# Optimization experiments

Measured on AMD Instinct MI355X. Metric: run time of the kernel, lower is better.

The kernel has to match this reference:

```python
import jax, jax.numpy as jnp
import numpy as np

B, S, D, H = 2, 1024, 1024, 16
DH = D // H
EPS = 1e-5

def _ln(x, g, b):
    m = jnp.mean(x, axis=-1, keepdims=True)
    v = jnp.mean((x - m) ** 2, axis=-1, keepdims=True)
    return (x - m) / jnp.sqrt(v + EPS) * g + b

def setup_inputs() -> dict:
    key = jax.random.key(0)
    ks = jax.random.split(key, 5)
    scale = 1.0 / np.sqrt(D)
    return {
        "id": jax.random.normal(ks[0], (B, S, D), dtype=jnp.float32),
        "Wq": jax.random.uniform(ks[1], (D, D), jnp.float32, -scale, scale),
        "Wk": jax.random.uniform(ks[2], (D, D), jnp.float32, -scale, scale),
        "Wv": jax.random.uniform(ks[3], (D, D), jnp.float32, -scale, scale),
        "g0": jnp.ones((D,), jnp.float32), "b0": jnp.zeros((D,), jnp.float32),
        "g1": jnp.ones((D,), jnp.float32), "b1": jnp.zeros((D,), jnp.float32),
        "g2": jnp.ones((D,), jnp.float32), "b2": jnp.zeros((D,), jnp.float32),
    }

def reference(id, Wq, Wk, Wv, g0, b0, g1, b1, g2, b2):
    residual = id
    id_ln = _ln(id, g0, b0)
    # torch Linear: x @ W.T ; split heads along last dim, cat along batch
    q = (id_ln @ Wq.T).reshape(B, S, H, DH)
    k = (id_ln @ Wk.T).reshape(B, S, H, DH)
    v = (id_ln @ Wv.T).reshape(B, S, H, DH)
    scores = jnp.einsum('bqhd,bkhd->bhqk', q, k) / np.sqrt(DH)
    A = jax.nn.softmax(scores, axis=-1)                      # [B,H,S,S]
    O = jnp.einsum('bhqk,bkhd->bqhd', A, v).reshape(B, S, D)  # merge heads
    left = _ln(id_ln + O, g1, b1)
    right = _ln(residual + O, g2, b2)
    out = left + right
    # torch layout of A is [(H*B), S, S] with head-major ordering
    A_out = jnp.transpose(A, (1, 0, 2, 3)).reshape(H * B, S, S)
    return (out, A_out)
```

## Files before the change

kernel.cpp:

```cpp
#include <hip/hip_runtime.h>

namespace {

constexpr int B = 2, S = 1024, D = 1024, H = 16, DH = 64;
constexpr int M = B * S;
constexpr float EPS = 1e-5f;

using bf16x8 = __attribute__((ext_vector_type(8))) short;
using bf16x4 = __attribute__((ext_vector_type(4))) short;
using f32x4  = __attribute__((ext_vector_type(4))) float;

typedef const __attribute__((address_space(1))) void* gptr_t;
typedef __attribute__((address_space(3))) void* lptr_t;

__device__ __forceinline__ unsigned short f2bf(float f) {
    union { float f; unsigned u; } v{f};
    unsigned r = v.u + 0x7fffu + ((v.u >> 16) & 1u);
    return (unsigned short)(r >> 16);
}

__device__ __forceinline__ float bflo(unsigned u) {
    union { unsigned u; float f; } v{u << 16}; return v.f;
}
__device__ __forceinline__ float bfhi(unsigned u) {
    union { unsigned u; float f; } v{u & 0xffff0000u}; return v.f;
}

__device__ __forceinline__ float wave_sum(float v) {
#pragma unroll
    for (int off = 32; off > 0; off >>= 1) v += __shfl_down(v, off, 64);
    return v;
}

__global__ __launch_bounds__(256) void cvt_w_kernel(
    const float* __restrict__ Wq, const float* __restrict__ Wk,
    const float* __restrict__ Wv, unsigned short* __restrict__ Wb)
{
    const float* src = (blockIdx.z == 0) ? Wq : (blockIdx.z == 1) ? Wk : Wv;
    const size_t i = ((size_t)blockIdx.x * 256 + threadIdx.x) * 4;
    float4 f = *reinterpret_cast<const float4*>(src + i);
    ushort4 h;
    h.x = f2bf(f.x); h.y = f2bf(f.y); h.z = f2bf(f.z); h.w = f2bf(f.w);
    *reinterpret_cast<ushort4*>(Wb + (size_t)blockIdx.z * D * D + i) = h;
}

__global__ __launch_bounds__(256) void ln0_kernel(
    const float* __restrict__ x, const float* __restrict__ g,
    const float* __restrict__ bt, float* __restrict__ y,
    unsigned short* __restrict__ yb)
{
    __shared__ float sm[8];
    __shared__ float stats[2];
    const int row = blockIdx.x;
    const int t = threadIdx.x;
    const float4 v = reinterpret_cast<const float4*>(x + (size_t)row * D)[t];
    float s  = v.x + v.y + v.z + v.w;
    float ss = v.x*v.x + v.y*v.y + v.z*v.z + v.w*v.w;
    s = wave_sum(s); ss = wave_sum(ss);
    const int lane = t & 63, wid = t >> 6;
    if (lane == 0) { sm[wid] = s; sm[4 + wid] = ss; }
    __syncthreads();
    if (t == 0) {
        float S1 = sm[0] + sm[1] + sm[2] + sm[3];
        float S2 = sm[4] + sm[5] + sm[6] + sm[7];
        float m  = S1 * (1.0f / D);
        float var = S2 * (1.0f / D) - m * m;
        stats[0] = m; stats[1] = rsqrtf(var + EPS);
    }
    __syncthreads();
    const float m = stats[0], r = stats[1];
    const float4 gv = reinterpret_cast<const float4*>(g)[t];
    const float4 bv = reinterpret_cast<const float4*>(bt)[t];
    float4 o;
    o.x = (v.x - m) * r * gv.x + bv.x;
    o.y = (v.y - m) * r * gv.y + bv.y;
    o.z = (v.z - m) * r * gv.z + bv.z;
    o.w = (v.w - m) * r * gv.w + bv.w;
    reinterpret_cast<float4*>(y + (size_t)row * D)[t] = o;
    ushort4 h; h.x = f2bf(o.x); h.y = f2bf(o.y); h.z = f2bf(o.z); h.w = f2bf(o.w);
    *reinterpret_cast<ushort4*>(yb + (size_t)row * D + t * 4) = h;
}

__global__ __launch_bounds__(256) void qkv_mfma_kernel(
    const unsigned short* __restrict__ idln, const unsigned short* __restrict__ Wb,
    unsigned short* __restrict__ q, unsigned short* __restrict__ k,
    unsigned short* __restrict__ vT)
{
    __shared__ unsigned short As[128 * 32];
    __shared__ unsigned short Bs[128 * 32];
    const int zi = blockIdx.z;
    const unsigned short* Bmat = Wb + (size_t)zi * D * D;
    const int m0 = blockIdx.y * 128, n0 = blockIdx.x * 128;
    const int t = threadIdx.x;
    const int w = t >> 6, lane = t & 63;
    const int wm = (w >> 1) * 64, wn = (w & 1) * 64;
    const int quad = lane >> 4, l16 = lane & 15;
    const int srow = t >> 2;
    const int scol = (t & 3) * 8;

    f32x4 acc[4][4];
#pragma unroll
    for (int i = 0; i < 4; ++i)
#pragma unroll
        for (int j = 0; j < 4; ++j) acc[i][j] = (f32x4){0.f, 0.f, 0.f, 0.f};

    for (int k0 = 0; k0 < D; k0 += 32) {
        __syncthreads();
#pragma unroll
        for (int c = 0; c < 2; ++c) {
            const unsigned short* ga = idln + (size_t)(m0 + srow + c * 64) * D + k0 + scol;
            __builtin_amdgcn_global_load_lds((gptr_t)ga, (lptr_t)(As + t * 8 + c * 2048), 16, 0, 0);
            const unsigned short* gb = Bmat + (size_t)(n0 + srow + c * 64) * D + k0 + scol;
            __builtin_amdgcn_global_load_lds((gptr_t)gb, (lptr_t)(Bs + t * 8 + c * 2048), 16, 0, 0);
        }
        __syncthreads();
        bf16x8 af[4], bfr[4];
#pragma unroll
        for (int i = 0; i < 4; ++i)
            af[i] = *reinterpret_cast<const bf16x8*>(As + (wm + i * 16 + l16) * 32 + quad * 8);
#pragma unroll
        for (int j = 0; j < 4; ++j)
            bfr[j] = *reinterpret_cast<const bf16x8*>(Bs + (wn + j * 16 + l16) * 32 + quad * 8);
#pragma unroll
        for (int i = 0; i < 4; ++i)
#pragma unroll
            for (int j = 0; j < 4; ++j)
                acc[i][j] = __builtin_amdgcn_mfma_f32_16x16x32_bf16(af[i], bfr[j], acc[i][j], 0, 0, 0);
    }

    if (zi < 2) {
        unsigned short* C = (zi == 0) ? q : k;
#pragma unroll
        for (int i = 0; i < 4; ++i)
#pragma unroll
            for (int j = 0; j < 4; ++j) {
                const int gcol = n0 + wn + j * 16 + l16;
#pragma unroll
                for (int reg = 0; reg < 4; ++reg) {
                    const int grow = m0 + wm + i * 16 + quad * 4 + reg;
                    C[(size_t)grow * D + gcol] = f2bf(acc[i][j][reg]);
                }
            }
    } else {
        const int b = m0 >> 10;
#pragma unroll
        for (int i = 0; i < 4; ++i)
#pragma unroll
            for (int j = 0; j < 4; ++j) {
                const int gcol = n0 + wn + j * 16 + l16;
                const int srow0 = (m0 - b * S) + wm + i * 16 + quad * 4;
                ushort4 h;
                h.x = f2bf(acc[i][j][0]); h.y = f2bf(acc[i][j][1]);
                h.z = f2bf(acc[i][j][2]); h.w = f2bf(acc[i][j][3]);
                *reinterpret_cast<ushort4*>(vT + ((size_t)b * D + gcol) * S + srow0) = h;
            }
    }
}

__global__ __launch_bounds__(256, 2) void attn_fused_kernel(
    const unsigned short* __restrict__ q, const unsigned short* __restrict__ k,
    const unsigned short* __restrict__ vT, float* __restrict__ Aout,
    float* __restrict__ O)
{
    __shared__ unsigned short Qs[2 * 64 * 32];
    __shared__ unsigned short Ks[2 * 64 * 32];
    __shared__ unsigned short Vs[4 * 64 * 16];

    const int z = blockIdx.z;
    const int b = z & 1, h = z >> 1;
    const int m0 = blockIdx.y * 64;
    const int t = threadIdx.x;
    const int w = t >> 6, lane = t & 63;
    const int quad = lane >> 4, l16 = lane & 15;
    const int sr = t >> 2, sc8 = (t & 3) * 8;

#pragma unroll
    for (int c = 0; c < 2; ++c) {
        const unsigned short* gq = q + (size_t)(b * S + m0 + sr) * D + h * DH + c * 32 + sc8;
        __builtin_amdgcn_global_load_lds((gptr_t)gq, (lptr_t)(Qs + c * 2048 + t * 8), 16, 0, 0);
    }
    __syncthreads();
    bf16x8 qf[2];
#pragma unroll
    for (int c = 0; c < 2; ++c)
        qf[c] = *reinterpret_cast<const bf16x8*>(Qs + c * 2048 + (w * 16 + l16) * 32 + quad * 8);

    f32x4 accO[4];
#pragma unroll
    for (int jj = 0; jj < 4; ++jj) accO[jj] = (f32x4){0.f, 0.f, 0.f, 0.f};
    float rsum = 0.f;
    uint2 pst[64];

#pragma unroll
    for (int tt = 0; tt < 16; ++tt) {
        const int n0 = tt * 64;
        __syncthreads();
#pragma unroll
        for (int c = 0; c < 2; ++c) {
            const unsigned short* gk = k + (size_t)(b * S + n0 + sr) * D + h * DH + c * 32 + sc8;
            __builtin_amdgcn_global_load_lds((gptr_t)gk, (lptr_t)(Ks + c * 2048 + t * 8), 16, 0, 0);
        }
#pragma unroll
        for (int c2 = 0; c2 < 2; ++c2) {
            const int kt = c2 * 2 + (t >> 7);
            const int dh = (t >> 1) & 63;
            const int kh = t & 1;
            const unsigned short* gv = vT + ((size_t)b * D + h * DH + dh) * S + n0 + kt * 16 + kh * 8;
            __builtin_amdgcn_global_load_lds((gptr_t)gv, (lptr_t)(Vs + c2 * 2048 + t * 8), 16, 0, 0);
        }
        __syncthreads();
#pragma unroll
        for (int kt = 0; kt < 4; ++kt) {
            f32x4 a = (f32x4){0.f, 0.f, 0.f, 0.f};
#pragma unroll
            for (int c = 0; c < 2; ++c) {
                bf16x8 kf = *reinterpret_cast<const bf16x8*>(Ks + c * 2048 + (kt * 16 + l16) * 32 + quad * 8);
                a = __builtin_amdgcn_mfma_f32_16x16x32_bf16(kf, qf[c], a, 0, 0, 0);
            }
            const float e0 = __expf(a[0] * 0.125f);
            const float e1 = __expf(a[1] * 0.125f);
            const float e2 = __expf(a[2] * 0.125f);
            const float e3 = __expf(a[3] * 0.125f);
            rsum += (e0 + e1) + (e2 + e3);
            bf16x4 p;
            p[0] = (short)f2bf(e0); p[1] = (short)f2bf(e1);
            p[2] = (short)f2bf(e2); p[3] = (short)f2bf(e3);
            pst[tt * 4 + kt] = *reinterpret_cast<uint2*>(&p);
#pragma unroll
            for (int jj = 0; jj < 4; ++jj) {
                bf16x4 vv = *reinterpret_cast<const bf16x4*>(Vs + kt * 1024 + (jj * 16 + l16) * 16 + quad * 4);
                accO[jj] = __builtin_amdgcn_mfma_f32_16x16x16bf16_1k(p, vv, accO[jj], 0, 0, 0);
            }
        }
    }

    rsum += __shfl_xor(rsum, 16, 64);
    rsum += __shfl_xor(rsum, 32, 64);
    const float sL = 1.0f / rsum;
    float sO[4];
#pragma unroll
    for (int r = 0; r < 4; ++r) sO[r] = __shfl(sL, quad * 4 + r, 64);

    float* Az = Aout + (size_t)z * S * S + (size_t)(m0 + w * 16 + l16) * S;
#pragma unroll
    for (int tt = 0; tt < 16; ++tt)
#pragma unroll
        for (int kt = 0; kt < 4; ++kt) {
            const uint2 u = pst[tt * 4 + kt];
            *reinterpret_cast<float4*>(Az + tt * 64 + kt * 16 + quad * 4) =
                make_float4(bflo(u.x) * sL, bfhi(u.x) * sL, bflo(u.y) * sL, bfhi(u.y) * sL);
        }

#pragma unroll
    for (int jj = 0; jj < 4; ++jj)
#pragma unroll
        for (int r = 0; r < 4; ++r) {
            const int grow = b * S + m0 + w * 16 + quad * 4 + r;
            O[(size_t)grow * D + h * DH + jj * 16 + l16] = accO[jj][r] * sO[r];
        }
}

__global__ __launch_bounds__(256) void final_kernel(
    const float* __restrict__ id, const float* __restrict__ id_ln, const float* __restrict__ O,
    const float* __restrict__ g1, const float* __restrict__ b1,
    const float* __restrict__ g2, const float* __restrict__ b2,
    float* __restrict__ out)
{
    __shared__ float sm[16];
    __shared__ float stats[4];
    const int row = blockIdx.x;
    const int t = threadIdx.x;
    const size_t base = (size_t)row * D;
    const float4 xi = reinterpret_cast<const float4*>(id + base)[t];
    const float4 xl = reinterpret_cast<const float4*>(id_ln + base)[t];
    const float4 xo = reinterpret_cast<const float4*>(O + base)[t];
    float4 t1, t2;
    t1.x = xl.x + xo.x; t1.y = xl.y + xo.y; t1.z = xl.z + xo.z; t1.w = xl.w + xo.w;
    t2.x = xi.x + xo.x; t2.y = xi.y + xo.y; t2.z = xi.z + xo.z; t2.w = xi.w + xo.w;
    float s1  = t1.x + t1.y + t1.z + t1.w;
    float ss1 = t1.x*t1.x + t1.y*t1.y + t1.z*t1.z + t1.w*t1.w;
    float s2  = t2.x + t2.y + t2.z + t2.w;
    float ss2 = t2.x*t2.x + t2.y*t2.y + t2.z*t2.z + t2.w*t2.w;
    s1 = wave_sum(s1); ss1 = wave_sum(ss1);
    s2 = wave_sum(s2); ss2 = wave_sum(ss2);
    const int lane = t & 63, wid = t >> 6;
    if (lane == 0) { sm[wid] = s1; sm[4+wid] = ss1; sm[8+wid] = s2; sm[12+wid] = ss2; }
    __syncthreads();
    if (t == 0) {
        float S1 = sm[0]+sm[1]+sm[2]+sm[3];
        float Q1 = sm[4]+sm[5]+sm[6]+sm[7];
        float S2 = sm[8]+sm[9]+sm[10]+sm[11];
        float Q2 = sm[12]+sm[13]+sm[14]+sm[15];
        float m1 = S1 * (1.0f / D);
        float m2 = S2 * (1.0f / D);
        stats[0] = m1; stats[1] = rsqrtf(Q1 * (1.0f / D) - m1*m1 + EPS);
        stats[2] = m2; stats[3] = rsqrtf(Q2 * (1.0f / D) - m2*m2 + EPS);
    }
    __syncthreads();
    const float m1 = stats[0], r1 = stats[1], m2 = stats[2], r2 = stats[3];
    const float4 g1v = reinterpret_cast<const float4*>(g1)[t];
    const float4 b1v = reinterpret_cast<const float4*>(b1)[t];
    const float4 g2v = reinterpret_cast<const float4*>(g2)[t];
    const float4 b2v = reinterpret_cast<const float4*>(b2)[t];
    float4 o;
    o.x = (t1.x - m1)*r1*g1v.x + b1v.x + (t2.x - m2)*r2*g2v.x + b2v.x;
    o.y = (t1.y - m1)*r1*g1v.y + b1v.y + (t2.y - m2)*r2*g2v.y + b2v.y;
    o.z = (t1.z - m1)*r1*g1v.z + b1v.z + (t2.z - m2)*r2*g2v.z + b2v.z;
    o.w = (t1.w - m1)*r1*g1v.w + b1v.w + (t2.w - m2)*r2*g2v.w + b2v.w;
    reinterpret_cast<float4*>(out + base)[t] = o;
}

}

extern "C" void kernel_launch(void* const* d_in, const int* in_sizes, int n_in,
                              void* d_out, int out_size, void* d_ws, size_t ws_size,
                              hipStream_t stream)
{
    const float* id = (const float*)d_in[0];
    const float* Wq = (const float*)d_in[1];
    const float* Wk = (const float*)d_in[2];
    const float* Wv = (const float*)d_in[3];
    const float* g0 = (const float*)d_in[4];
    const float* b0 = (const float*)d_in[5];
    const float* g1 = (const float*)d_in[6];
    const float* b1 = (const float*)d_in[7];
    const float* g2 = (const float*)d_in[8];
    const float* b2 = (const float*)d_in[9];

    float* out  = (float*)d_out;
    float* Aout = out + (size_t)B * S * D;

    char* ws = (char*)d_ws;
    float* id_ln  = (float*)(ws);
    float* O      = (float*)(ws + (8u << 20));
    unsigned short* idln_bf = (unsigned short*)(ws + (16u << 20));
    unsigned short* Wb      = idln_bf + (size_t)M * D;
    unsigned short* qb      = Wb + (size_t)3 * D * D;
    unsigned short* kb      = qb + (size_t)M * D;
    unsigned short* vT      = kb + (size_t)M * D;

    hipLaunchKernelGGL(cvt_w_kernel, dim3(D * D / 1024, 1, 3), dim3(256), 0, stream,
                       Wq, Wk, Wv, Wb);
    hipLaunchKernelGGL(ln0_kernel, dim3(M), dim3(256), 0, stream, id, g0, b0, id_ln, idln_bf);
    hipLaunchKernelGGL(qkv_mfma_kernel, dim3(D / 128, M / 128, 3), dim3(256), 0, stream,
                       idln_bf, Wb, qb, kb, vT);
    hipLaunchKernelGGL(attn_fused_kernel, dim3(1, S / 64, H * B), dim3(256), 0, stream,
                       qb, kb, vT, Aout, O);
    hipLaunchKernelGGL(final_kernel, dim3(M), dim3(256), 0, stream,
                       id, id_ln, O, g1, b1, g2, b2, out);
}
```

Baseline: 240.9 us.

## Double-buffer K/V tiles in attention, merge prep kernels, shrink QKV M-tile

The attention kernel now keeps two K/V shared-memory buffers and issues the load for the next 64-key tile before computing on the current one, so each step needs one barrier and fetch latency can overlap MFMA work. The weight-conversion and LayerNorm0 kernels are merged into a single launch, with block index choosing which job a block does. The QKV GEMM M-tile shrinks from 128 to 64 rows, which doubles the grid for better CU occupancy but reduces reuse of each weight tile. Double buffering doubles the K/V LDS footprint, which could limit the two-blocks-per-CU occupancy target.

```diff
diff --git a/kernel.cpp b/kernel.cpp
--- a/kernel.cpp
+++ b/kernel.cpp
@@ -32,27 +32,28 @@
     return v;
 }
 
-__global__ __launch_bounds__(256) void cvt_w_kernel(
+__global__ __launch_bounds__(256) void pre_kernel(
     const float* __restrict__ Wq, const float* __restrict__ Wk,
-    const float* __restrict__ Wv, unsigned short* __restrict__ Wb)
-{
-    const float* src = (blockIdx.z == 0) ? Wq : (blockIdx.z == 1) ? Wk : Wv;
-    const size_t i = ((size_t)blockIdx.x * 256 + threadIdx.x) * 4;
-    float4 f = *reinterpret_cast<const float4*>(src + i);
-    ushort4 h;
-    h.x = f2bf(f.x); h.y = f2bf(f.y); h.z = f2bf(f.z); h.w = f2bf(f.w);
-    *reinterpret_cast<ushort4*>(Wb + (size_t)blockIdx.z * D * D + i) = h;
-}
-
-__global__ __launch_bounds__(256) void ln0_kernel(
+    const float* __restrict__ Wv, unsigned short* __restrict__ Wb,
     const float* __restrict__ x, const float* __restrict__ g,
     const float* __restrict__ bt, float* __restrict__ y,
     unsigned short* __restrict__ yb)
 {
+    const int bx = blockIdx.x;
+    const int t = threadIdx.x;
+    if (bx < 3072) {
+        const int z = bx >> 10;
+        const float* src = (z == 0) ? Wq : (z == 1) ? Wk : Wv;
+        const size_t i = ((size_t)(bx & 1023) * 256 + t) * 4;
+        float4 f = *reinterpret_cast<const float4*>(src + i);
+        ushort4 h;
+        h.x = f2bf(f.x); h.y = f2bf(f.y); h.z = f2bf(f.z); h.w = f2bf(f.w);
+        *reinterpret_cast<ushort4*>(Wb + (size_t)z * D * D + i) = h;
+        return;
+    }
     __shared__ float sm[8];
     __shared__ float stats[2];
-    const int row = blockIdx.x;
-    const int t = threadIdx.x;
+    const int row = bx - 3072;
     const float4 v = reinterpret_cast<const float4*>(x + (size_t)row * D)[t];
     float s  = v.x + v.y + v.z + v.w;
     float ss = v.x*v.x + v.y*v.y + v.z*v.z + v.w*v.w;
@@ -86,43 +87,45 @@
     unsigned short* __restrict__ q, unsigned short* __restrict__ k,
     unsigned short* __restrict__ vT)
 {
-    __shared__ unsigned short As[128 * 32];
+    __shared__ unsigned short As[64 * 32];
     __shared__ unsigned short Bs[128 * 32];
     const int zi = blockIdx.z;
     const unsigned short* Bmat = Wb + (size_t)zi * D * D;
-    const int m0 = blockIdx.y * 128, n0 = blockIdx.x * 128;
+    const int m0 = blockIdx.y * 64, n0 = blockIdx.x * 128;
     const int t = threadIdx.x;
     const int w = t >> 6, lane = t & 63;
-    const int wm = (w >> 1) * 64, wn = (w & 1) * 64;
+    const int wm = (w >> 1) * 32, wn = (w & 1) * 64;
     const int quad = lane >> 4, l16 = lane & 15;
     const int srow = t >> 2;
     const int scol = (t & 3) * 8;
 
-    f32x4 acc[4][4];
-#pragma unroll
-    for (int i = 0; i < 4; ++i)
+    f32x4 acc[2][4];
+#pragma unroll
+    for (int i = 0; i < 2; ++i)
 #pragma unroll
         for (int j = 0; j < 4; ++j) acc[i][j] = (f32x4){0.f, 0.f, 0.f, 0.f};
 
     for (int k0 = 0; k0 < D; k0 += 32) {
         __syncthreads();
+        {
+            const unsigned short* ga = idln + (size_t)(m0 + srow) * D + k0 + scol;
+            __builtin_amdgcn_global_load_lds((gptr_t)ga, (lptr_t)(As + t * 8), 16, 0, 0);
+        }
 #pragma unroll
         for (int c = 0; c < 2; ++c) {
-            const unsigned short* ga = idln + (size_t)(m0 + srow + c * 64) * D + k0 + scol;
-            __builtin_amdgcn_global_load_lds((gptr_t)ga, (lptr_t)(As + t * 8 + c * 2048), 16, 0, 0);
             const unsigned short* gb = Bmat + (size_t)(n0 + srow + c * 64) * D + k0 + scol;
             __builtin_amdgcn_global_load_lds((gptr_t)gb, (lptr_t)(Bs + t * 8 + c * 2048), 16, 0, 0);
         }
         __syncthreads();
-        bf16x8 af[4], bfr[4];
-#pragma unroll
-        for (int i = 0; i < 4; ++i)
+        bf16x8 af[2], bfr[4];
+#pragma unroll
+        for (int i = 0; i < 2; ++i)
             af[i] = *reinterpret_cast<const bf16x8*>(As + (wm + i * 16 + l16) * 32 + quad * 8);
 #pragma unroll
         for (int j = 0; j < 4; ++j)
             bfr[j] = *reinterpret_cast<const bf16x8*>(Bs + (wn + j * 16 + l16) * 32 + quad * 8);
 #pragma unroll
-        for (int i = 0; i < 4; ++i)
+        for (int i = 0; i < 2; ++i)
 #pragma unroll
             for (int j = 0; j < 4; ++j)
                 acc[i][j] = __builtin_amdgcn_mfma_f32_16x16x32_bf16(af[i], bfr[j], acc[i][j], 0, 0, 0);
@@ -131,7 +134,7 @@
     if (zi < 2) {
         unsigned short* C = (zi == 0) ? q : k;
 #pragma unroll
-        for (int i = 0; i < 4; ++i)
+        for (int i = 0; i < 2; ++i)
 #pragma unroll
             for (int j = 0; j < 4; ++j) {
                 const int gcol = n0 + wn + j * 16 + l16;
@@ -144,7 +147,7 @@
     } else {
         const int b = m0 >> 10;
 #pragma unroll
-        for (int i = 0; i < 4; ++i)
+        for (int i = 0; i < 2; ++i)
 #pragma unroll
             for (int j = 0; j < 4; ++j) {
                 const int gcol = n0 + wn + j * 16 + l16;
@@ -163,8 +166,8 @@
     float* __restrict__ O)
 {
     __shared__ unsigned short Qs[2 * 64 * 32];
-    __shared__ unsigned short Ks[2 * 64 * 32];
-    __shared__ unsigned short Vs[4 * 64 * 16];
+    __shared__ unsigned short Ks[2][2 * 64 * 32];
+    __shared__ unsigned short Vs[2][4 * 64 * 16];
 
     const int z = blockIdx.z;
     const int b = z & 1, h = z >> 1;
@@ -174,31 +177,11 @@
     const int quad = lane >> 4, l16 = lane & 15;
     const int sr = t >> 2, sc8 = (t & 3) * 8;
 
-#pragma unroll
-    for (int c = 0; c < 2; ++c) {
-        const unsigned short* gq = q + (size_t)(b * S + m0 + sr) * D + h * DH + c * 32 + sc8;
-        __builtin_amdgcn_global_load_lds((gptr_t)gq, (lptr_t)(Qs + c * 2048 + t * 8), 16, 0, 0);
-    }
-    __syncthreads();
-    bf16x8 qf[2];
-#pragma unroll
-    for (int c = 0; c < 2; ++c)
-        qf[c] = *reinterpret_cast<const bf16x8*>(Qs + c * 2048 + (w * 16 + l16) * 32 + quad * 8);
-
-    f32x4 accO[4];
-#pragma unroll
-    for (int jj = 0; jj < 4; ++jj) accO[jj] = (f32x4){0.f, 0.f, 0.f, 0.f};
-    float rsum = 0.f;
-    uint2 pst[64];
-
-#pragma unroll
-    for (int tt = 0; tt < 16; ++tt) {
-        const int n0 = tt * 64;
-        __syncthreads();
+    auto STAGE = [&](int n0, int bb) {
 #pragma unroll
         for (int c = 0; c < 2; ++c) {
             const unsigned short* gk = k + (size_t)(b * S + n0 + sr) * D + h * DH + c * 32 + sc8;
-            __builtin_amdgcn_global_load_lds((gptr_t)gk, (lptr_t)(Ks + c * 2048 + t * 8), 16, 0, 0);
+            __builtin_amdgcn_global_load_lds((gptr_t)gk, (lptr_t)(Ks[bb] + c * 2048 + t * 8), 16, 0, 0);
         }
 #pragma unroll
         for (int c2 = 0; c2 < 2; ++c2) {
@@ -206,15 +189,38 @@
             const int dh = (t >> 1) & 63;
             const int kh = t & 1;
             const unsigned short* gv = vT + ((size_t)b * D + h * DH + dh) * S + n0 + kt * 16 + kh * 8;
-            __builtin_amdgcn_global_load_lds((gptr_t)gv, (lptr_t)(Vs + c2 * 2048 + t * 8), 16, 0, 0);
-        }
-        __syncthreads();
+            __builtin_amdgcn_global_load_lds((gptr_t)gv, (lptr_t)(Vs[bb] + c2 * 2048 + t * 8), 16, 0, 0);
+        }
+    };
+
+#pragma unroll
+    for (int c = 0; c < 2; ++c) {
+        const unsigned short* gq = q + (size_t)(b * S + m0 + sr) * D + h * DH + c * 32 + sc8;
+        __builtin_amdgcn_global_load_lds((gptr_t)gq, (lptr_t)(Qs + c * 2048 + t * 8), 16, 0, 0);
+    }
+    STAGE(0, 0);
+    __syncthreads();
+    bf16x8 qf[2];
+#pragma unroll
+    for (int c = 0; c < 2; ++c)
+        qf[c] = *reinterpret_cast<const bf16x8*>(Qs + c * 2048 + (w * 16 + l16) * 32 + quad * 8);
+
+    f32x4 accO[4];
+#pragma unroll
+    for (int jj = 0; jj < 4; ++jj) accO[jj] = (f32x4){0.f, 0.f, 0.f, 0.f};
+    float rsum = 0.f;
+    uint2 pst[64];
+    int cur = 0;
+
+#pragma unroll
+    for (int tt = 0; tt < 16; ++tt) {
+        if (tt < 15) STAGE((tt + 1) * 64, cur ^ 1);
 #pragma unroll
         for (int kt = 0; kt < 4; ++kt) {
             f32x4 a = (f32x4){0.f, 0.f, 0.f, 0.f};
 #pragma unroll
             for (int c = 0; c < 2; ++c) {
-                bf16x8 kf = *reinterpret_cast<const bf16x8*>(Ks + c * 2048 + (kt * 16 + l16) * 32 + quad * 8);
+                bf16x8 kf = *reinterpret_cast<const bf16x8*>(Ks[cur] + c * 2048 + (kt * 16 + l16) * 32 + quad * 8);
                 a = __builtin_amdgcn_mfma_f32_16x16x32_bf16(kf, qf[c], a, 0, 0, 0);
             }
             const float e0 = __expf(a[0] * 0.125f);
@@ -228,10 +234,12 @@
             pst[tt * 4 + kt] = *reinterpret_cast<uint2*>(&p);
 #pragma unroll
             for (int jj = 0; jj < 4; ++jj) {
-                bf16x4 vv = *reinterpret_cast<const bf16x4*>(Vs + kt * 1024 + (jj * 16 + l16) * 16 + quad * 4);
+                bf16x4 vv = *reinterpret_cast<const bf16x4*>(Vs[cur] + kt * 1024 + (jj * 16 + l16) * 16 + quad * 4);
                 accO[jj] = __builtin_amdgcn_mfma_f32_16x16x16bf16_1k(p, vv, accO[jj], 0, 0, 0);
             }
         }
+        __syncthreads();
+        cur ^= 1;
     }
 
     rsum += __shfl_xor(rsum, 16, 64);
@@ -339,10 +347,9 @@
     unsigned short* kb      = qb + (size_t)M * D;
     unsigned short* vT      = kb + (size_t)M * D;
 
-    hipLaunchKernelGGL(cvt_w_kernel, dim3(D * D / 1024, 1, 3), dim3(256), 0, stream,
-                       Wq, Wk, Wv, Wb);
-    hipLaunchKernelGGL(ln0_kernel, dim3(M), dim3(256), 0, stream, id, g0, b0, id_ln, idln_bf);
-    hipLaunchKernelGGL(qkv_mfma_kernel, dim3(D / 128, M / 128, 3), dim3(256), 0, stream,
+    hipLaunchKernelGGL(pre_kernel, dim3(3072 + M), dim3(256), 0, stream,
+                       Wq, Wk, Wv, Wb, id, g0, b0, id_ln, idln_bf);
+    hipLaunchKernelGGL(qkv_mfma_kernel, dim3(D / 128, M / 64, 3), dim3(256), 0, stream,
                        idln_bf, Wb, qb, kb, vT);
     hipLaunchKernelGGL(attn_fused_kernel, dim3(1, S / 64, H * B), dim3(256), 0, stream,
                        qb, kb, vT, Aout, O);
```

Measured after the change: 267.8 us. 11.1% more time.
